# Kernel tuning notes

Hardware: AMD Instinct MI355X
Metric: run time of the kernel (lower is better)

Reference implementation:

```python
import jax, jax.numpy as jnp
import numpy as np

N_NODES = 50000
N_EDGES = 500000
N_GRAPHS = 64
IN_DIM = 64
HID = 128
N_LAYERS = 2
BN_EPS = 1e-5


def setup_inputs() -> dict:
    key = jax.random.key(0)
    ks = jax.random.split(key, 12)
    x = jax.random.normal(ks[0], (N_NODES, IN_DIM), dtype=jnp.float32)
    edge_index = jax.random.randint(ks[1], (2, N_EDGES), 0, N_NODES, dtype=jnp.int64)
    batch = jnp.sort(jax.random.randint(ks[2], (N_NODES,), 0, N_GRAPHS, dtype=jnp.int64))
    s = 0.05
    W_enc = jax.random.normal(ks[3], (IN_DIM, HID), dtype=jnp.float32) * s
    b_enc = jnp.zeros((HID,), dtype=jnp.float32)
    Wc = jax.random.normal(ks[4], (N_LAYERS, HID, HID), dtype=jnp.float32) * s
    bc = jnp.zeros((N_LAYERS, HID), dtype=jnp.float32)
    gamma = jnp.ones((N_LAYERS, HID), dtype=jnp.float32)
    beta = jnp.zeros((N_LAYERS, HID), dtype=jnp.float32)
    MID = HID // 2
    W1 = jax.random.normal(ks[5], (HID, MID), dtype=jnp.float32) * s
    b1 = jnp.zeros((MID,), dtype=jnp.float32)
    W2 = jax.random.normal(ks[6], (MID, 1), dtype=jnp.float32) * s
    b2 = jnp.zeros((1,), dtype=jnp.float32)
    return {"x": x, "edge_index": edge_index, "batch": batch,
            "W_enc": W_enc, "b_enc": b_enc, "Wc": Wc, "bc": bc,
            "gamma": gamma, "beta": beta, "W1": W1, "b1": b1,
            "W2": W2, "b2": b2}


def _gcn_conv(h, src, dst, norm, W, b, n_nodes):
    # h: [N, HID]; src/dst: [E+N] (self-loops included); norm: [E+N]
    h = h @ W                                   # [N, HID]
    msg = h[src] * norm[:, None]                # gather + normalize
    out = jax.ops.segment_sum(msg, dst, num_segments=n_nodes)  # scatter-add
    return out + b


def _batch_norm(h, g, b):
    mu = jnp.mean(h, axis=0)
    var = jnp.var(h, axis=0)
    return (h - mu) * jax.lax.rsqrt(var + BN_EPS) * g + b


def reference(x, edge_index, batch, W_enc, b_enc, Wc, bc, gamma, beta, W1, b1, W2, b2):
    n = x.shape[0]
    loop = jnp.arange(n, dtype=edge_index.dtype)
    src = jnp.concatenate([edge_index[0], loop])   # [E+N]
    dst = jnp.concatenate([edge_index[1], loop])
    # symmetric GCN normalization with self-loops: deg over target index
    deg = jax.ops.segment_sum(jnp.ones_like(dst, dtype=x.dtype), dst, num_segments=n)
    dinv = jax.lax.rsqrt(deg)                      # deg >= 1 due to self-loops
    norm = dinv[src] * dinv[dst]                   # [E+N]

    h = x @ W_enc + b_enc                          # node encoder
    for l in range(Wc.shape[0]):
        h = _gcn_conv(h, src, dst, norm, Wc[l], bc[l], n)
        h = _batch_norm(h, gamma[l], beta[l])
        h = jax.nn.relu(h)                         # dropout inactive (eval)

    # global mean pool over graphs
    pooled = jax.ops.segment_sum(h, batch, num_segments=N_GRAPHS)
    counts = jax.ops.segment_sum(jnp.ones((n,), dtype=h.dtype), batch, num_segments=N_GRAPHS)
    pooled = pooled / jnp.maximum(counts, 1.0)[:, None]

    z = jax.nn.relu(pooled @ W1 + b1)
    out = jax.nn.sigmoid(z @ W2 + b2)              # [B, 1]
    return out.squeeze(-1)                          # [B]
```

## Files before the change

### kernel.cpp

```cpp
#include <hip/hip_runtime.h>
#include <hip/hip_bf16.h>
#include <hip/hip_fp16.h>
#include <math.h>


typedef _Float16 f16x8 __attribute__((ext_vector_type(8)));
typedef float f32x4 __attribute__((ext_vector_type(4)));

__device__ inline unsigned pack2(float a, float b) {
  union { __half2 h; unsigned u; } p;
  p.h = __floats2half2_rn(a, b);
  return p.u;
}
__device__ inline float2 unpack2(unsigned u) {
  union { unsigned u; __half2 h; } p;
  p.u = u;
  return __half22float2(p.h);
}

__global__ __launch_bounds__(256) void k_setup(
    int* __restrict__ deg, float* __restrict__ bnstat, int statTotal,
    float* __restrict__ pooled, int N, int nbN,
    const float* __restrict__ W_enc, const float* __restrict__ b_enc,
    const float* __restrict__ Wc, unsigned short* __restrict__ MT,
    float* __restrict__ bfold, int NL,
    const float* __restrict__ Wc1, unsigned short* __restrict__ WT1,
    const int* __restrict__ batch, int* __restrict__ gstart) {
  int b = blockIdx.x;
  if (b < nbN) {
    int i = b * 256 + threadIdx.x;
    if (i < N) deg[i] = 1;
    if (i < statTotal) bnstat[i] = 0.f;
    if (i < 64 * 128) pooled[i] = 0.f;
    return;
  }
  b -= nbN;
  if (b < 65) {
    if (threadIdx.x < 128) {
      int n = threadIdx.x;
      int k = b;
      const float* arow = (k < 64) ? (W_enc + (size_t)k * 128) : b_enc;
      float acc = 0.f;
      for (int j = 0; j < 128; j++)
        acc = fmaf(arow[j], Wc[(size_t)j * 128 + n], acc);
      if (k < 64) ((__half*)MT)[(size_t)n * 64 + k] = __float2half(acc);
      else bfold[n] = acc;
    }
    return;
  }
  b -= 65;
  if (b < 64) {
    if (NL > 1) {
      int i = b * 256 + threadIdx.x;
      int n = i & 127, k = i >> 7;
      ((__half*)WT1)[(size_t)n * 128 + k] = __float2half(Wc1[i]);
    }
    return;
  }
  int g = threadIdx.x;
  if (g <= 64) {
    int lo = 0, hi = N;
    while (lo < hi) {
      int mid = (lo + hi) >> 1;
      if (batch[mid] < g) lo = mid + 1;
      else hi = mid;
    }
    gstart[g] = lo;
  }
}

__global__ __launch_bounds__(256) void k_deg(const int* __restrict__ ei, int E,
                                             int* __restrict__ deg) {
  int i = blockIdx.x * 256 + threadIdx.x;
  if (i < E) atomicAdd(&deg[ei[E + i]], 1);
}

__global__ __launch_bounds__(256) void k_scan_a(const int* __restrict__ deg, int N,
                                                int* __restrict__ rowptr,
                                                int* __restrict__ blksum) {
  __shared__ int s[256];
  int t = threadIdx.x;
  int i = blockIdx.x * 256 + t;
  int v = (i < N) ? deg[i] : 0;
  s[t] = v;
  __syncthreads();
  for (int off = 1; off < 256; off <<= 1) {
    int x = (t >= off) ? s[t - off] : 0;
    __syncthreads();
    s[t] += x;
    __syncthreads();
  }
  if (i < N) rowptr[i] = s[t] - v;
  if (t == 255) blksum[blockIdx.x] = s[255];
}

__global__ __launch_bounds__(256) void k_scan_c(const int* __restrict__ deg, int N,
                                                int total,
                                                const int* __restrict__ blksum,
                                                int* __restrict__ rowptr,
                                                int* __restrict__ cursor,
                                                float* __restrict__ dinv) {
  __shared__ int red[256];
  int t = threadIdx.x, b = blockIdx.x;
  int acc = 0;
  for (int j = t; j < b; j += 256) acc += blksum[j];
  red[t] = acc;
  __syncthreads();
  for (int off = 128; off > 0; off >>= 1) {
    if (t < off) red[t] += red[t + off];
    __syncthreads();
  }
  int prefix = red[0];
  int i = b * 256 + t;
  if (i < N) {
    int rp = rowptr[i] + prefix;
    rowptr[i] = rp;
    cursor[i] = rp;
    dinv[i] = rsqrtf((float)deg[i]);
  } else if (i == N) {
    rowptr[N] = total;
  }
}

__global__ __launch_bounds__(256) void k_fillprep(
    const int* __restrict__ ei, int E, int N, int nbEN,
    int* __restrict__ cursor, int* __restrict__ colx,
    const float* __restrict__ x, const float* __restrict__ dinv,
    unsigned* __restrict__ xs2) {
  int b = blockIdx.x;
  if (b < nbEN) {
    int i = b * 256 + threadIdx.x;
    if (i < E) {
      int s = ei[i];
      int d = ei[E + i];
      int pos = atomicAdd(&cursor[d], 1);
      colx[pos] = s;
    } else if (i < E + N) {
      int j = i - E;
      int pos = atomicAdd(&cursor[j], 1);
      colx[pos] = j;
    }
    return;
  }
  b -= nbEN;
  int i = b * 256 + threadIdx.x;
  if (i < N * 16) {
    int row = i >> 4;
    float4 v = ((const float4*)x)[i];
    float d = dinv[row];
    uint2 o;
    o.x = pack2(v.x * d, v.y * d);
    o.y = pack2(v.z * d, v.w * d);
    ((uint2*)xs2)[i] = o;
  }
}

__global__ __launch_bounds__(256, 4) void k_aggemm0(
    const uint2* __restrict__ xs, const int* __restrict__ rowptr,
    const int* __restrict__ colx, const float* __restrict__ dinv,
    const unsigned short* __restrict__ MT,
    const float* __restrict__ bias,
    const float* __restrict__ bias2,
    float* __restrict__ stat,
    unsigned short* __restrict__ Yh, int N) {
  constexpr int KP = 68;
  __shared__ unsigned short Al[32 * KP];
  __shared__ float wvl[32];
  __shared__ float red[2][2][128];

  int lane = threadIdx.x & 63;
  int wv = threadIdx.x >> 6;
  int grp = lane >> 4, l16 = lane & 15;
  int rowBlk = blockIdx.x * 32;

#pragma unroll 1
  for (int it = 0; it < 2; it++) {
    int lr = it * 16 + wv * 4 + grp;
    int i = rowBlk + lr;
    float s0 = 0.f, s1 = 0.f, s2 = 0.f, s3 = 0.f, sd = 0.f;
    if (i < N) {
      int beg = rowptr[i], end = rowptr[i + 1];
      int e = beg;
#pragma unroll 1
      for (; e + 8 <= end; e += 8) {
        int ix[8];
#pragma unroll
        for (int u = 0; u < 8; u++) ix[u] = colx[e + u];
        uint2 v[8];
        float dd[8];
#pragma unroll
        for (int u = 0; u < 8; u++) { v[u] = xs[(size_t)ix[u] * 16 + l16]; dd[u] = dinv[ix[u]]; }
#pragma unroll
        for (int u = 0; u < 8; u++) {
          float2 a = unpack2(v[u].x), b = unpack2(v[u].y);
          s0 += a.x; s1 += a.y; s2 += b.x; s3 += b.y;
          sd += dd[u];
        }
      }
#pragma unroll 1
      for (; e < end; e++) {
        int sr = colx[e];
        uint2 vv = xs[(size_t)sr * 16 + l16];
        float2 a = unpack2(vv.x), b = unpack2(vv.y);
        s0 += a.x; s1 += a.y; s2 += b.x; s3 += b.y;
        sd += dinv[sr];
      }
    }
    float di = (i < N) ? dinv[i] : 0.f;
    *(uint2*)&Al[lr * KP + l16 * 4] =
        make_uint2(pack2(s0 * di, s1 * di), pack2(s2 * di, s3 * di));
    if (l16 == 0) wvl[lr] = di * sd;
  }
  __syncthreads();

  int l15 = lane & 15;
  int kg = lane >> 4;
  int wr = wv & 1, wc = wv >> 1;
  f16x8 af[2];
#pragma unroll
  for (int j = 0; j < 2; j++)
    af[j] = *(const f16x8*)&Al[(wr * 16 + l15) * KP + kg * 8 + j * 32];

  f32x4 acc[4];
#pragma unroll
  for (int t = 0; t < 4; t++) acc[t] = {0.f, 0.f, 0.f, 0.f};
#pragma unroll
  for (int j = 0; j < 2; j++) {
#pragma unroll
    for (int t = 0; t < 4; t++) {
      f16x8 bf = *(const f16x8*)&MT[(size_t)(wc * 64 + t * 16 + l15) * 64 + kg * 8 + j * 32];
      acc[t] = __builtin_amdgcn_mfma_f32_16x16x32_f16(af[j], bf, acc[t], 0, 0, 0);
    }
  }

  int rbaseL = wr * 16 + kg * 4;
  int rbase = rowBlk + rbaseL;
  float wrow[4];
#pragma unroll
  for (int r = 0; r < 4; r++) wrow[r] = wvl[rbaseL + r];

#pragma unroll
  for (int t = 0; t < 4; t++) {
    int ch = wc * 64 + t * 16 + l15;
    float bb = bias[ch];
    float b2v = bias2[ch];
    float s = 0.f, q = 0.f;
#pragma unroll
    for (int r = 0; r < 4; r++) {
      int row = rbase + r;
      if (row < N) {
        float o = fmaf(wrow[r], b2v, acc[t][r] + bb);
        __half oh = __float2half(o);
        Yh[(size_t)row * 128 + ch] = *(unsigned short*)&oh;
        s += o;
        q += o * o;
      }
    }
    s += __shfl_xor(s, 16); s += __shfl_xor(s, 32);
    q += __shfl_xor(q, 16); q += __shfl_xor(q, 32);
    if (kg == 0) { red[wr][0][ch] = s; red[wr][1][ch] = q; }
  }
  __syncthreads();
  int st = threadIdx.x >> 7, ch2 = threadIdx.x & 127;
  float v = red[0][st][ch2] + red[1][st][ch2];
  atomicAdd(&stat[(blockIdx.x & 7) * 256 + st * 128 + ch2], v);
}

__global__ __launch_bounds__(256, 4) void k_aggemm1(
    const unsigned short* __restrict__ Hprev,
    const int* __restrict__ rowptr, const int* __restrict__ colx,
    const float* __restrict__ dinv,
    const unsigned short* __restrict__ WT,
    const float* __restrict__ statPrev, const float* __restrict__ gamma,
    const float* __restrict__ beta, float invN,
    const float* __restrict__ bias,
    float* __restrict__ statCur, unsigned short* __restrict__ Yh, int N) {
  constexpr int KP = 136;
  __shared__ unsigned short Al[32 * KP];
  __shared__ float scsh[256];
  __shared__ float red[2][2][128];

  if (threadIdx.x < 128) {
    int c = threadIdx.x;
    float ss = 0.f, qs = 0.f;
#pragma unroll
    for (int r = 0; r < 8; r++) {
      ss += statPrev[r * 256 + c];
      qs += statPrev[r * 256 + 128 + c];
    }
    float mu = ss * invN;
    float var = qs * invN - mu * mu;
    float sc = rsqrtf(var + 1e-5f) * gamma[c];
    scsh[c] = sc;
    scsh[128 + c] = beta[c] - mu * sc;
  }
  __syncthreads();

  int lane = threadIdx.x & 63;
  int wv = threadIdx.x >> 6;
  int half = lane >> 5, l32 = lane & 31;
  int rowBlk = blockIdx.x * 32;
  const uint2* Hp = (const uint2*)Hprev;
  float4 sc = ((const float4*)scsh)[l32];
  float4 sh = ((const float4*)(scsh + 128))[l32];

#pragma unroll 1
  for (int it = 0; it < 4; it++) {
    int lr = it * 8 + wv * 2 + half;
    int i = rowBlk + lr;
    float4 s = make_float4(0.f, 0.f, 0.f, 0.f);
    if (i < N) {
      int beg = rowptr[i], end = rowptr[i + 1];
      int e = beg;
#pragma unroll 1
      for (; e + 8 <= end; e += 8) {
        int ix[8];
#pragma unroll
        for (int u = 0; u < 8; u++) ix[u] = colx[e + u];
        uint2 v[8];
        float dd[8];
#pragma unroll
        for (int u = 0; u < 8; u++) { v[u] = Hp[(size_t)ix[u] * 32 + l32]; dd[u] = dinv[ix[u]]; }
#pragma unroll
        for (int u = 0; u < 8; u++) {
          float2 a = unpack2(v[u].x), b = unpack2(v[u].y);
          s.x += fmaxf(fmaf(a.x, sc.x, sh.x), 0.f) * dd[u];
          s.y += fmaxf(fmaf(a.y, sc.y, sh.y), 0.f) * dd[u];
          s.z += fmaxf(fmaf(b.x, sc.z, sh.z), 0.f) * dd[u];
          s.w += fmaxf(fmaf(b.y, sc.w, sh.w), 0.f) * dd[u];
        }
      }
#pragma unroll 1
      for (; e < end; e++) {
        int sr = colx[e];
        uint2 vv = Hp[(size_t)sr * 32 + l32];
        float dsr = dinv[sr];
        float2 a = unpack2(vv.x), b = unpack2(vv.y);
        s.x += fmaxf(fmaf(a.x, sc.x, sh.x), 0.f) * dsr;
        s.y += fmaxf(fmaf(a.y, sc.y, sh.y), 0.f) * dsr;
        s.z += fmaxf(fmaf(b.x, sc.z, sh.z), 0.f) * dsr;
        s.w += fmaxf(fmaf(b.y, sc.w, sh.w), 0.f) * dsr;
      }
    }
    float di = (i < N) ? dinv[i] : 0.f;
    *(uint2*)&Al[lr * KP + l32 * 4] =
        make_uint2(pack2(s.x * di, s.y * di), pack2(s.z * di, s.w * di));
  }
  __syncthreads();

  int l15 = lane & 15;
  int kg = lane >> 4;
  int wr = wv & 1, wc = wv >> 1;
  f16x8 af[4];
#pragma unroll
  for (int j = 0; j < 4; j++)
    af[j] = *(const f16x8*)&Al[(wr * 16 + l15) * KP + kg * 8 + j * 32];

  f32x4 acc[4];
#pragma unroll
  for (int t = 0; t < 4; t++) acc[t] = {0.f, 0.f, 0.f, 0.f};
#pragma unroll
  for (int j = 0; j < 4; j++) {
#pragma unroll
    for (int t = 0; t < 4; t++) {
      f16x8 bf = *(const f16x8*)&WT[(size_t)(wc * 64 + t * 16 + l15) * 128 + kg * 8 + j * 32];
      acc[t] = __builtin_amdgcn_mfma_f32_16x16x32_f16(af[j], bf, acc[t], 0, 0, 0);
    }
  }

  int rbase = rowBlk + wr * 16 + kg * 4;
#pragma unroll
  for (int t = 0; t < 4; t++) {
    int ch = wc * 64 + t * 16 + l15;
    float bb = bias[ch];
    float s = 0.f, q = 0.f;
#pragma unroll
    for (int r = 0; r < 4; r++) {
      int row = rbase + r;
      if (row < N) {
        float o = acc[t][r] + bb;
        __half oh = __float2half(o);
        Yh[(size_t)row * 128 + ch] = *(unsigned short*)&oh;
        s += o;
        q += o * o;
      }
    }
    s += __shfl_xor(s, 16); s += __shfl_xor(s, 32);
    q += __shfl_xor(q, 16); q += __shfl_xor(q, 32);
    if (kg == 0) { red[wr][0][ch] = s; red[wr][1][ch] = q; }
  }
  __syncthreads();
  int st = threadIdx.x >> 7, ch2 = threadIdx.x & 127;
  float v = red[0][st][ch2] + red[1][st][ch2];
  atomicAdd(&statCur[(blockIdx.x & 7) * 256 + st * 128 + ch2], v);
}

__global__ __launch_bounds__(256) void k_wprep(const float* __restrict__ Wsrc,
                                               unsigned short* __restrict__ WT) {
  int i = blockIdx.x * 256 + threadIdx.x;
  int n = i & 127, k = i >> 7;
  ((__half*)WT)[(size_t)n * 128 + k] = __float2half(Wsrc[i]);
}

__global__ __launch_bounds__(256) void k_pool(
    const unsigned* __restrict__ H16u,
    const float* __restrict__ stat, const float* __restrict__ gamma,
    const float* __restrict__ beta, float invN,
    const int* __restrict__ gstart, float* __restrict__ pooled) {
  __shared__ float scsh[256];
  __shared__ float red[4][128];
  if (threadIdx.x < 128) {
    int c = threadIdx.x;
    float ss = 0.f, qs = 0.f;
#pragma unroll
    for (int r = 0; r < 8; r++) {
      ss += stat[r * 256 + c];
      qs += stat[r * 256 + 128 + c];
    }
    float mu = ss * invN;
    float var = qs * invN - mu * mu;
    float sc = rsqrtf(var + 1e-5f) * gamma[c];
    scsh[c] = sc;
    scsh[128 + c] = beta[c] - mu * sc;
  }
  __syncthreads();

  int g = blockIdx.x >> 3;
  int part = blockIdx.x & 7;
  int beg = gstart[g], end = gstart[g + 1];
  int len = end - beg;
  int p0 = beg + (len * part) / 8;
  int p1 = beg + (len * (part + 1)) / 8;

  int l64 = threadIdx.x & 63;
  int rs = threadIdx.x >> 6;
  int c0 = l64 * 2;
  float sc0 = scsh[c0], sc1 = scsh[c0 + 1];
  float sh0 = scsh[128 + c0], sh1 = scsh[128 + c0 + 1];
  int plen = p1 - p0;
  int q0 = p0 + (plen * rs) / 4;
  int q1 = p0 + (plen * (rs + 1)) / 4;

  float a0 = 0.f, a1 = 0.f;
  for (int r = q0; r < q1; r++) {
    float2 f = unpack2(H16u[(size_t)r * 64 + l64]);
    a0 += fmaxf(fmaf(f.x, sc0, sh0), 0.f);
    a1 += fmaxf(fmaf(f.y, sc1, sh1), 0.f);
  }
  red[rs][c0] = a0;
  red[rs][c0 + 1] = a1;
  __syncthreads();
  if (threadIdx.x < 128) {
    float s = red[0][threadIdx.x] + red[1][threadIdx.x] +
              red[2][threadIdx.x] + red[3][threadIdx.x];
    atomicAdd(&pooled[g * 128 + threadIdx.x], s);
  }
}

__global__ __launch_bounds__(256) void k_mlp(const float* __restrict__ pooled,
                                             const int* __restrict__ gstart,
                                             const float* __restrict__ W1,
                                             const float* __restrict__ b1,
                                             const float* __restrict__ W2,
                                             const float* __restrict__ b2,
                                             float* __restrict__ out) {
  __shared__ float P[64 * 128];
  __shared__ float Z[64 * 64];
  for (int i = threadIdx.x; i < 64 * 128; i += 256) {
    int g = i >> 7;
    int cnt = gstart[g + 1] - gstart[g];
    P[i] = pooled[i] / (float)(cnt > 1 ? cnt : 1);
  }
  __syncthreads();
  for (int i = threadIdx.x; i < 64 * 64; i += 256) {
    int g = i >> 6, m = i & 63;
    float acc = b1[m];
    for (int k = 0; k < 128; k++) acc += P[(g << 7) + k] * W1[k * 64 + m];
    Z[i] = fmaxf(acc, 0.f);
  }
  __syncthreads();
  if (threadIdx.x < 64) {
    int g = threadIdx.x;
    float acc = b2[0];
    for (int m = 0; m < 64; m++) acc += Z[(g << 6) + m] * W2[m];
    out[g] = 1.f / (1.f + expf(-acc));
  }
}


extern "C" void kernel_launch(void* const* d_in, const int* in_sizes, int n_in,
                              void* d_out, int out_size, void* d_ws, size_t ws_size,
                              hipStream_t stream) {
  const float* x      = (const float*)d_in[0];
  const int*   ei     = (const int*)d_in[1];
  const int*   batch  = (const int*)d_in[2];
  const float* W_enc  = (const float*)d_in[3];
  const float* b_enc  = (const float*)d_in[4];
  const float* Wc     = (const float*)d_in[5];
  const float* bc     = (const float*)d_in[6];
  const float* gamma  = (const float*)d_in[7];
  const float* beta   = (const float*)d_in[8];
  const float* W1     = (const float*)d_in[9];
  const float* b1     = (const float*)d_in[10];
  const float* W2     = (const float*)d_in[11];
  const float* b2     = (const float*)d_in[12];
  float* out = (float*)d_out;

  const int N = in_sizes[2];
  const int E = in_sizes[1] / 2;
  const int NL = in_sizes[6] / 128;

  size_t off = 0;
  auto alloc = [&](size_t bytes) {
    void* p = (char*)d_ws + off;
    off += (bytes + 255) & ~(size_t)255;
    return p;
  };
  unsigned short* h16a = (unsigned short*)alloc((size_t)N * 128 * 2);
  unsigned short* h16b = (unsigned short*)alloc((size_t)N * 128 * 2);
  int*   deg    = (int*)alloc((size_t)N * 4);
  float* dinv   = (float*)alloc((size_t)N * 4);
  int*   rowptr = (int*)alloc((size_t)(N + 1) * 4);
  int*   cursor = (int*)alloc((size_t)N * 4);
  int*   colx   = (int*)alloc((size_t)(E + N) * 4);
  int*   blksum = (int*)alloc(1024 * 4);
  float* bnstat = (float*)alloc((size_t)NL * 2048 * 4);
  float* pooled = (float*)alloc(64 * 128 * 4);
  int*   gstart = (int*)alloc(65 * 4);
  unsigned short* MT  = (unsigned short*)alloc(128 * 64 * 2);
  unsigned short* WT1 = (unsigned short*)alloc(128 * 128 * 2);
  float* bfold  = (float*)alloc(128 * 4);
  unsigned* xs  = (unsigned*)alloc((size_t)N * 64 * 2);

  int nbN = (N + 255) / 256;
  int nbEN = (E + N + 255) / 256;
  float invN = 1.f / (float)N;
  int tiles32 = (N + 31) / 32;

  k_setup<<<nbN + 130, 256, 0, stream>>>(
      deg, bnstat, NL * 2048, pooled, N, nbN, W_enc, b_enc, Wc, MT, bfold, NL,
      Wc + (size_t)128 * 128, WT1, batch, gstart);
  k_deg<<<(E + 255) / 256, 256, 0, stream>>>(ei, E, deg);
  k_scan_a<<<nbN, 256, 0, stream>>>(deg, N, rowptr, blksum);
  k_scan_c<<<nbN, 256, 0, stream>>>(deg, N, E + N, blksum, rowptr, cursor, dinv);
  k_fillprep<<<nbEN + (N * 16 + 255) / 256, 256, 0, stream>>>(
      ei, E, N, nbEN, cursor, colx, x, dinv, xs);

  k_aggemm0<<<tiles32, 256, 0, stream>>>((const uint2*)xs, rowptr, colx, dinv,
                                         MT, bc, bfold, bnstat, h16a, N);

  unsigned short* cur = h16a;
  unsigned short* nxt = h16b;
  for (int l = 1; l < NL; l++) {
    if (l > 1)
      k_wprep<<<64, 256, 0, stream>>>(Wc + (size_t)l * 128 * 128, WT1);
    k_aggemm1<<<tiles32, 256, 0, stream>>>(
        cur, rowptr, colx, dinv, WT1, bnstat + (l - 1) * 2048,
        gamma + (l - 1) * 128, beta + (l - 1) * 128, invN, bc + l * 128,
        bnstat + l * 2048, nxt, N);
    unsigned short* tmp = cur; cur = nxt; nxt = tmp;
  }

  k_pool<<<64 * 8, 256, 0, stream>>>((const unsigned*)cur,
                                     bnstat + (NL - 1) * 2048,
                                     gamma + (NL - 1) * 128,
                                     beta + (NL - 1) * 128, invN, gstart,
                                     pooled);
  k_mlp<<<1, 256, 0, stream>>>(pooled, gstart, W1, b1, W2, b2, out);
}
```

Measured before the change: 258.5 us.

## Merge graph-build kernels into one cooperative kernel and widen gather loads

Replaces the setup, degree, two scan and fill kernels with a single cooperative kernel of 512 blocks that separates phases with grid-wide syncs, removing several launch gaps. The aggregation kernels now gather 16-byte rows per lane instead of 8-byte rows, so fewer lanes cover each row and more rows are processed concurrently per wave; the LDS row pitch is changed to keep 16-byte alignment. Risks: grid.sync overhead, lower parallelism in the build phases with only 512 blocks, and more registers per thread in the gather loops.

New measurement: 516.2 us. 2x slower.

```diff
diff --git a/kernel.cpp b/kernel.cpp
--- a/kernel.cpp
+++ b/kernel.cpp
@@ -1,7 +1,10 @@
 #include <hip/hip_runtime.h>
 #include <hip/hip_bf16.h>
 #include <hip/hip_fp16.h>
+#include <hip/hip_cooperative_groups.h>
 #include <math.h>
+
+namespace cg = cooperative_groups;
 
 
 typedef _Float16 f16x8 __attribute__((ext_vector_type(8)));
@@ -18,166 +21,160 @@
   return __half22float2(p.h);
 }
 
-__global__ __launch_bounds__(256) void k_setup(
-    int* __restrict__ deg, float* __restrict__ bnstat, int statTotal,
-    float* __restrict__ pooled, int N, int nbN,
-    const float* __restrict__ W_enc, const float* __restrict__ b_enc,
-    const float* __restrict__ Wc, unsigned short* __restrict__ MT,
-    float* __restrict__ bfold, int NL,
-    const float* __restrict__ Wc1, unsigned short* __restrict__ WT1,
-    const int* __restrict__ batch, int* __restrict__ gstart) {
-  int b = blockIdx.x;
-  if (b < nbN) {
-    int i = b * 256 + threadIdx.x;
-    if (i < N) deg[i] = 1;
-    if (i < statTotal) bnstat[i] = 0.f;
-    if (i < 64 * 128) pooled[i] = 0.f;
-    return;
-  }
-  b -= nbN;
-  if (b < 65) {
-    if (threadIdx.x < 128) {
-      int n = threadIdx.x;
-      int k = b;
-      const float* arow = (k < 64) ? (W_enc + (size_t)k * 128) : b_enc;
-      float acc = 0.f;
-      for (int j = 0; j < 128; j++)
-        acc = fmaf(arow[j], Wc[(size_t)j * 128 + n], acc);
-      if (k < 64) ((__half*)MT)[(size_t)n * 64 + k] = __float2half(acc);
-      else bfold[n] = acc;
-    }
-    return;
-  }
-  b -= 65;
-  if (b < 64) {
-    if (NL > 1) {
-      int i = b * 256 + threadIdx.x;
+struct BuildArgs {
+  int* deg;
+  float* bnstat;
+  int statTotal;
+  float* pooled;
+  int N, E;
+  const float* W_enc;
+  const float* b_enc;
+  const float* Wc;
+  unsigned short* MT;
+  float* bfold;
+  int NL;
+  const float* Wc1;
+  unsigned short* WT1;
+  const int* batch;
+  int* gstart;
+  const int* ei;
+  int* rowptr;
+  int* blksum;
+  int* cursor;
+  float* dinv;
+  int* colx;
+  const float* x;
+  unsigned* xs;
+};
+
+__global__ __launch_bounds__(256) void k_build(BuildArgs a) {
+  cg::grid_group grid = cg::this_grid();
+  __shared__ int s[256];
+  int t = threadIdx.x;
+  int tid = blockIdx.x * 256 + t;
+  int nthr = gridDim.x * 256;
+  int N = a.N, E = a.E;
+
+  for (int i = tid; i < N; i += nthr) a.deg[i] = 1;
+  for (int i = tid; i < a.statTotal; i += nthr) a.bnstat[i] = 0.f;
+  for (int i = tid; i < 64 * 128; i += nthr) a.pooled[i] = 0.f;
+  for (int i = tid; i < 65 * 128; i += nthr) {
+    int k = i >> 7, n = i & 127;
+    const float* arow = (k < 64) ? (a.W_enc + (size_t)k * 128) : a.b_enc;
+    float acc = 0.f;
+    for (int j = 0; j < 128; j++)
+      acc = fmaf(arow[j], a.Wc[(size_t)j * 128 + n], acc);
+    if (k < 64) ((__half*)a.MT)[(size_t)n * 64 + k] = __float2half(acc);
+    else a.bfold[n] = acc;
+  }
+  if (a.NL > 1) {
+    for (int i = tid; i < 128 * 128; i += nthr) {
       int n = i & 127, k = i >> 7;
-      ((__half*)WT1)[(size_t)n * 128 + k] = __float2half(Wc1[i]);
-    }
-    return;
-  }
-  int g = threadIdx.x;
-  if (g <= 64) {
-    int lo = 0, hi = N;
+      ((__half*)a.WT1)[(size_t)n * 128 + k] = __float2half(a.Wc1[i]);
+    }
+  }
+  if (tid <= 64) {
+    int g = tid, lo = 0, hi = N;
     while (lo < hi) {
       int mid = (lo + hi) >> 1;
-      if (batch[mid] < g) lo = mid + 1;
+      if (a.batch[mid] < g) lo = mid + 1;
       else hi = mid;
     }
-    gstart[g] = lo;
-  }
-}
-
-__global__ __launch_bounds__(256) void k_deg(const int* __restrict__ ei, int E,
-                                             int* __restrict__ deg) {
-  int i = blockIdx.x * 256 + threadIdx.x;
-  if (i < E) atomicAdd(&deg[ei[E + i]], 1);
-}
-
-__global__ __launch_bounds__(256) void k_scan_a(const int* __restrict__ deg, int N,
-                                                int* __restrict__ rowptr,
-                                                int* __restrict__ blksum) {
-  __shared__ int s[256];
-  int t = threadIdx.x;
-  int i = blockIdx.x * 256 + t;
-  int v = (i < N) ? deg[i] : 0;
-  s[t] = v;
-  __syncthreads();
-  for (int off = 1; off < 256; off <<= 1) {
-    int x = (t >= off) ? s[t - off] : 0;
+    a.gstart[g] = lo;
+  }
+  grid.sync();
+
+  for (int i = tid; i < E; i += nthr) atomicAdd(&a.deg[a.ei[E + i]], 1);
+  grid.sync();
+
+  int nchunks = (N + 255) / 256;
+  for (int c = blockIdx.x; c < nchunks; c += gridDim.x) {
+    int i = c * 256 + t;
+    int v = (i < N) ? a.deg[i] : 0;
+    s[t] = v;
     __syncthreads();
-    s[t] += x;
+    for (int off = 1; off < 256; off <<= 1) {
+      int xx = (t >= off) ? s[t - off] : 0;
+      __syncthreads();
+      s[t] += xx;
+      __syncthreads();
+    }
+    if (i < N) a.rowptr[i] = s[t] - v;
+    if (t == 255) a.blksum[c] = s[255];
     __syncthreads();
   }
-  if (i < N) rowptr[i] = s[t] - v;
-  if (t == 255) blksum[blockIdx.x] = s[255];
-}
-
-__global__ __launch_bounds__(256) void k_scan_c(const int* __restrict__ deg, int N,
-                                                int total,
-                                                const int* __restrict__ blksum,
-                                                int* __restrict__ rowptr,
-                                                int* __restrict__ cursor,
-                                                float* __restrict__ dinv) {
-  __shared__ int red[256];
-  int t = threadIdx.x, b = blockIdx.x;
-  int acc = 0;
-  for (int j = t; j < b; j += 256) acc += blksum[j];
-  red[t] = acc;
-  __syncthreads();
-  for (int off = 128; off > 0; off >>= 1) {
-    if (t < off) red[t] += red[t + off];
+  grid.sync();
+
+  for (int c = blockIdx.x; c < nchunks; c += gridDim.x) {
+    int acc = 0;
+    for (int j = t; j < c; j += 256) acc += a.blksum[j];
+    s[t] = acc;
     __syncthreads();
-  }
-  int prefix = red[0];
-  int i = b * 256 + t;
-  if (i < N) {
-    int rp = rowptr[i] + prefix;
-    rowptr[i] = rp;
-    cursor[i] = rp;
-    dinv[i] = rsqrtf((float)deg[i]);
-  } else if (i == N) {
-    rowptr[N] = total;
-  }
-}
-
-__global__ __launch_bounds__(256) void k_fillprep(
-    const int* __restrict__ ei, int E, int N, int nbEN,
-    int* __restrict__ cursor, int* __restrict__ colx,
-    const float* __restrict__ x, const float* __restrict__ dinv,
-    unsigned* __restrict__ xs2) {
-  int b = blockIdx.x;
-  if (b < nbEN) {
-    int i = b * 256 + threadIdx.x;
+    for (int off = 128; off > 0; off >>= 1) {
+      if (t < off) s[t] += s[t + off];
+      __syncthreads();
+    }
+    int prefix = s[0];
+    __syncthreads();
+    int i = c * 256 + t;
+    if (i < N) {
+      int rp = a.rowptr[i] + prefix;
+      a.rowptr[i] = rp;
+      a.cursor[i] = rp;
+      a.dinv[i] = rsqrtf((float)a.deg[i]);
+    } else if (i == N) {
+      a.rowptr[N] = E + N;
+    }
+  }
+  grid.sync();
+
+  for (int i = tid; i < E + N; i += nthr) {
     if (i < E) {
-      int s = ei[i];
-      int d = ei[E + i];
-      int pos = atomicAdd(&cursor[d], 1);
-      colx[pos] = s;
-    } else if (i < E + N) {
+      int sr = a.ei[i];
+      int d = a.ei[E + i];
+      int pos = atomicAdd(&a.cursor[d], 1);
+      a.colx[pos] = sr;
+    } else {
       int j = i - E;
-      int pos = atomicAdd(&cursor[j], 1);
-      colx[pos] = j;
-    }
-    return;
-  }
-  b -= nbEN;
-  int i = b * 256 + threadIdx.x;
-  if (i < N * 16) {
+      int pos = atomicAdd(&a.cursor[j], 1);
+      a.colx[pos] = j;
+    }
+  }
+  for (int i = tid; i < N * 16; i += nthr) {
     int row = i >> 4;
-    float4 v = ((const float4*)x)[i];
-    float d = dinv[row];
+    float4 v = ((const float4*)a.x)[i];
+    float d = a.dinv[row];
     uint2 o;
     o.x = pack2(v.x * d, v.y * d);
     o.y = pack2(v.z * d, v.w * d);
-    ((uint2*)xs2)[i] = o;
+    ((uint2*)a.xs)[i] = o;
   }
 }
 
 __global__ __launch_bounds__(256, 4) void k_aggemm0(
-    const uint2* __restrict__ xs, const int* __restrict__ rowptr,
-    const int* __restrict__ colx, const float* __restrict__ dinv,
+    const uint4* __restrict__ xs4,
+    const int* __restrict__ rowptr, const int* __restrict__ colx,
+    const float* __restrict__ dinv,
     const unsigned short* __restrict__ MT,
     const float* __restrict__ bias,
     const float* __restrict__ bias2,
     float* __restrict__ stat,
     unsigned short* __restrict__ Yh, int N) {
-  constexpr int KP = 68;
+  constexpr int KP = 72;
   __shared__ unsigned short Al[32 * KP];
   __shared__ float wvl[32];
   __shared__ float red[2][2][128];
 
   int lane = threadIdx.x & 63;
   int wv = threadIdx.x >> 6;
-  int grp = lane >> 4, l16 = lane & 15;
+  int g8 = lane >> 3, l8 = lane & 7;
   int rowBlk = blockIdx.x * 32;
 
-#pragma unroll 1
-  for (int it = 0; it < 2; it++) {
-    int lr = it * 16 + wv * 4 + grp;
+  {
+    int lr = wv * 8 + g8;
     int i = rowBlk + lr;
-    float s0 = 0.f, s1 = 0.f, s2 = 0.f, s3 = 0.f, sd = 0.f;
+    float s0 = 0.f, s1 = 0.f, s2 = 0.f, s3 = 0.f;
+    float s4 = 0.f, s5 = 0.f, s6 = 0.f, s7 = 0.f, sd = 0.f;
     if (i < N) {
       int beg = rowptr[i], end = rowptr[i + 1];
       int e = beg;
@@ -186,30 +183,38 @@
         int ix[8];
 #pragma unroll
         for (int u = 0; u < 8; u++) ix[u] = colx[e + u];
-        uint2 v[8];
+        uint4 v[8];
         float dd[8];
 #pragma unroll
-        for (int u = 0; u < 8; u++) { v[u] = xs[(size_t)ix[u] * 16 + l16]; dd[u] = dinv[ix[u]]; }
+        for (int u = 0; u < 8; u++) { v[u] = xs4[(size_t)ix[u] * 8 + l8]; dd[u] = dinv[ix[u]]; }
 #pragma unroll
         for (int u = 0; u < 8; u++) {
-          float2 a = unpack2(v[u].x), b = unpack2(v[u].y);
-          s0 += a.x; s1 += a.y; s2 += b.x; s3 += b.y;
+          float2 p0 = unpack2(v[u].x), p1 = unpack2(v[u].y);
+          float2 p2 = unpack2(v[u].z), p3 = unpack2(v[u].w);
+          s0 += p0.x; s1 += p0.y; s2 += p1.x; s3 += p1.y;
+          s4 += p2.x; s5 += p2.y; s6 += p3.x; s7 += p3.y;
           sd += dd[u];
         }
       }
 #pragma unroll 1
       for (; e < end; e++) {
         int sr = colx[e];
-        uint2 vv = xs[(size_t)sr * 16 + l16];
-        float2 a = unpack2(vv.x), b = unpack2(vv.y);
-        s0 += a.x; s1 += a.y; s2 += b.x; s3 += b.y;
+        uint4 v = xs4[(size_t)sr * 8 + l8];
+        float2 p0 = unpack2(v.x), p1 = unpack2(v.y);
+        float2 p2 = unpack2(v.z), p3 = unpack2(v.w);
+        s0 += p0.x; s1 += p0.y; s2 += p1.x; s3 += p1.y;
+        s4 += p2.x; s5 += p2.y; s6 += p3.x; s7 += p3.y;
         sd += dinv[sr];
       }
     }
     float di = (i < N) ? dinv[i] : 0.f;
-    *(uint2*)&Al[lr * KP + l16 * 4] =
-        make_uint2(pack2(s0 * di, s1 * di), pack2(s2 * di, s3 * di));
-    if (l16 == 0) wvl[lr] = di * sd;
+    uint4 o;
+    o.x = pack2(s0 * di, s1 * di);
+    o.y = pack2(s2 * di, s3 * di);
+    o.z = pack2(s4 * di, s5 * di);
+    o.w = pack2(s6 * di, s7 * di);
+    *(uint4*)&Al[lr * KP + l8 * 8] = o;
+    if (l8 == 0) wvl[lr] = di * sd;
   }
   __syncthreads();
 
@@ -298,17 +303,20 @@
 
   int lane = threadIdx.x & 63;
   int wv = threadIdx.x >> 6;
-  int half = lane >> 5, l32 = lane & 31;
+  int grp = lane >> 4, l16 = lane & 15;
   int rowBlk = blockIdx.x * 32;
-  const uint2* Hp = (const uint2*)Hprev;
-  float4 sc = ((const float4*)scsh)[l32];
-  float4 sh = ((const float4*)(scsh + 128))[l32];
+  const uint4* Hp4 = (const uint4*)Hprev;
+  float4 scA = ((const float4*)scsh)[l16 * 2];
+  float4 scB = ((const float4*)scsh)[l16 * 2 + 1];
+  float4 shA = ((const float4*)(scsh + 128))[l16 * 2];
+  float4 shB = ((const float4*)(scsh + 128))[l16 * 2 + 1];
 
 #pragma unroll 1
-  for (int it = 0; it < 4; it++) {
-    int lr = it * 8 + wv * 2 + half;
+  for (int it = 0; it < 2; it++) {
+    int lr = it * 16 + wv * 4 + grp;
     int i = rowBlk + lr;
-    float4 s = make_float4(0.f, 0.f, 0.f, 0.f);
+    float s0 = 0.f, s1 = 0.f, s2 = 0.f, s3 = 0.f;
+    float s4 = 0.f, s5 = 0.f, s6 = 0.f, s7 = 0.f;
     if (i < N) {
       int beg = rowptr[i], end = rowptr[i + 1];
       int e = beg;
@@ -317,34 +325,49 @@
         int ix[8];
 #pragma unroll
         for (int u = 0; u < 8; u++) ix[u] = colx[e + u];
-        uint2 v[8];
+        uint4 v[8];
         float dd[8];
 #pragma unroll
-        for (int u = 0; u < 8; u++) { v[u] = Hp[(size_t)ix[u] * 32 + l32]; dd[u] = dinv[ix[u]]; }
+        for (int u = 0; u < 8; u++) { v[u] = Hp4[(size_t)ix[u] * 16 + l16]; dd[u] = dinv[ix[u]]; }
 #pragma unroll
         for (int u = 0; u < 8; u++) {
-          float2 a = unpack2(v[u].x), b = unpack2(v[u].y);
-          s.x += fmaxf(fmaf(a.x, sc.x, sh.x), 0.f) * dd[u];
-          s.y += fmaxf(fmaf(a.y, sc.y, sh.y), 0.f) * dd[u];
-          s.z += fmaxf(fmaf(b.x, sc.z, sh.z), 0.f) * dd[u];
-          s.w += fmaxf(fmaf(b.y, sc.w, sh.w), 0.f) * dd[u];
+          float2 p0 = unpack2(v[u].x), p1 = unpack2(v[u].y);
+          float2 p2 = unpack2(v[u].z), p3 = unpack2(v[u].w);
+          float d = dd[u];
+          s0 += fmaxf(fmaf(p0.x, scA.x, shA.x), 0.f) * d;
+          s1 += fmaxf(fmaf(p0.y, scA.y, shA.y), 0.f) * d;
+          s2 += fmaxf(fmaf(p1.x, scA.z, shA.z), 0.f) * d;
+          s3 += fmaxf(fmaf(p1.y, scA.w, shA.w), 0.f) * d;
+          s4 += fmaxf(fmaf(p2.x, scB.x, shB.x), 0.f) * d;
+          s5 += fmaxf(fmaf(p2.y, scB.y, shB.y), 0.f) * d;
+          s6 += fmaxf(fmaf(p3.x, scB.z, shB.z), 0.f) * d;
+          s7 += fmaxf(fmaf(p3.y, scB.w, shB.w), 0.f) * d;
         }
       }
 #pragma unroll 1
       for (; e < end; e++) {
         int sr = colx[e];
-        uint2 vv = Hp[(size_t)sr * 32 + l32];
-        float dsr = dinv[sr];
-        float2 a = unpack2(vv.x), b = unpack2(vv.y);
-        s.x += fmaxf(fmaf(a.x, sc.x, sh.x), 0.f) * dsr;
-        s.y += fmaxf(fmaf(a.y, sc.y, sh.y), 0.f) * dsr;
-        s.z += fmaxf(fmaf(b.x, sc.z, sh.z), 0.f) * dsr;
-        s.w += fmaxf(fmaf(b.y, sc.w, sh.w), 0.f) * dsr;
+        uint4 v = Hp4[(size_t)sr * 16 + l16];
+        float d = dinv[sr];
+        float2 p0 = unpack2(v.x), p1 = unpack2(v.y);
+        float2 p2 = unpack2(v.z), p3 = unpack2(v.w);
+        s0 += fmaxf(fmaf(p0.x, scA.x, shA.x), 0.f) * d;
+        s1 += fmaxf(fmaf(p0.y, scA.y, shA.y), 0.f) * d;
+        s2 += fmaxf(fmaf(p1.x, scA.z, shA.z), 0.f) * d;
+        s3 += fmaxf(fmaf(p1.y, scA.w, shA.w), 0.f) * d;
+        s4 += fmaxf(fmaf(p2.x, scB.x, shB.x), 0.f) * d;
+        s5 += fmaxf(fmaf(p2.y, scB.y, shB.y), 0.f) * d;
+        s6 += fmaxf(fmaf(p3.x, scB.z, shB.z), 0.f) * d;
+        s7 += fmaxf(fmaf(p3.y, scB.w, shB.w), 0.f) * d;
       }
     }
     float di = (i < N) ? dinv[i] : 0.f;
-    *(uint2*)&Al[lr * KP + l32 * 4] =
-        make_uint2(pack2(s.x * di, s.y * di), pack2(s.z * di, s.w * di));
+    uint4 o;
+    o.x = pack2(s0 * di, s1 * di);
+    o.y = pack2(s2 * di, s3 * di);
+    o.z = pack2(s4 * di, s5 * di);
+    o.w = pack2(s6 * di, s7 * di);
+    *(uint4*)&Al[lr * KP + l16 * 8] = o;
   }
   __syncthreads();
 
@@ -532,21 +555,25 @@
   float* bfold  = (float*)alloc(128 * 4);
   unsigned* xs  = (unsigned*)alloc((size_t)N * 64 * 2);
 
-  int nbN = (N + 255) / 256;
-  int nbEN = (E + N + 255) / 256;
   float invN = 1.f / (float)N;
   int tiles32 = (N + 31) / 32;
 
-  k_setup<<<nbN + 130, 256, 0, stream>>>(
-      deg, bnstat, NL * 2048, pooled, N, nbN, W_enc, b_enc, Wc, MT, bfold, NL,
-      Wc + (size_t)128 * 128, WT1, batch, gstart);
-  k_deg<<<(E + 255) / 256, 256, 0, stream>>>(ei, E, deg);
-  k_scan_a<<<nbN, 256, 0, stream>>>(deg, N, rowptr, blksum);
-  k_scan_c<<<nbN, 256, 0, stream>>>(deg, N, E + N, blksum, rowptr, cursor, dinv);
-  k_fillprep<<<nbEN + (N * 16 + 255) / 256, 256, 0, stream>>>(
-      ei, E, N, nbEN, cursor, colx, x, dinv, xs);
-
-  k_aggemm0<<<tiles32, 256, 0, stream>>>((const uint2*)xs, rowptr, colx, dinv,
+  BuildArgs ba;
+  ba.deg = deg; ba.bnstat = bnstat; ba.statTotal = NL * 2048;
+  ba.pooled = pooled; ba.N = N; ba.E = E;
+  ba.W_enc = W_enc; ba.b_enc = b_enc; ba.Wc = Wc;
+  ba.MT = MT; ba.bfold = bfold; ba.NL = NL;
+  ba.Wc1 = Wc + (size_t)128 * 128; ba.WT1 = WT1;
+  ba.batch = batch; ba.gstart = gstart;
+  ba.ei = ei; ba.rowptr = rowptr; ba.blksum = blksum;
+  ba.cursor = cursor; ba.dinv = dinv; ba.colx = colx;
+  ba.x = x; ba.xs = xs;
+
+  void* kargs[] = {&ba};
+  hipLaunchCooperativeKernel((void*)k_build, dim3(512), dim3(256), kargs, 0,
+                             stream);
+
+  k_aggemm0<<<tiles32, 256, 0, stream>>>((const uint4*)xs, rowptr, colx, dinv,
                                          MT, bc, bfold, bnstat, h16a, N);
 
   unsigned short* cur = h16a;
```
